# Performance work log

Hardware: AMD Instinct MI355X
Metric: run time of the kernel (lower is better)

Reference implementation:

```python
import jax, jax.numpy as jnp
import numpy as np

N = 50000      # nodes
E = 800000     # edges (avg degree 16)
DIN = 256      # input_dim
DH = 128       # hidden_dim
ALPHA_LOGIT = 0.6190392084062235  # logit(0.65)


def setup_inputs() -> dict:
    key = jax.random.key(0)
    ks = jax.random.split(key, 12)
    f = lambda k, s: jax.random.normal(k, s, dtype=jnp.float32)
    return {
        "x": f(ks[0], (N, DIN)),
        "edge_index": jax.random.randint(ks[1], (2, E), 0, N, dtype=jnp.int32),
        "reranker_scores": f(ks[2], (N,)),
        # input_proj
        "Wp": f(ks[3], (DIN, DH)) * 0.02, "bp": jnp.zeros((DH,), jnp.float32),
        # SAGEConv 0: lin_l (aggregated neighbors, with bias), lin_r (root, no bias)
        "Wl0": f(ks[4], (DIN, DH)) * 0.02, "bl0": jnp.zeros((DH,), jnp.float32),
        "Wr0": f(ks[5], (DIN, DH)) * 0.02,
        # SAGEConv 1
        "Wl1": f(ks[6], (DH, DH)) * 0.02, "bl1": jnp.zeros((DH,), jnp.float32),
        "Wr1": f(ks[7], (DH, DH)) * 0.02,
        # score head MLP
        "W1": f(ks[8], (DH, DH // 2)) * 0.02, "b1": jnp.zeros((DH // 2,), jnp.float32),
        "W2": f(ks[9], (DH // 2, 1)) * 0.02, "b2": jnp.zeros((1,), jnp.float32),
        "alpha_logit": jnp.float32(ALPHA_LOGIT),
    }


def _sage_conv(h, src, dst, Wl, bl, Wr):
    # PyG SAGEConv (aggr='mean', root_weight=True):
    # out = lin_l(mean_{j in N(i)} h_j) + lin_r(h_i)
    msg = h[src]                                             # [E, d] gather
    agg = jax.ops.segment_sum(msg, dst, num_segments=N)      # [N, d]
    cnt = jax.ops.segment_sum(jnp.ones((src.shape[0],), h.dtype), dst, num_segments=N)
    agg = agg / jnp.maximum(cnt, 1.0)[:, None]               # mean; isolated nodes -> 0
    return agg @ Wl + bl + h @ Wr


def reference(x, edge_index, reranker_scores, Wp, bp, Wl0, bl0, Wr0,
              Wl1, bl1, Wr1, W1, b1, W2, b2, alpha_logit):
    src, dst = edge_index[0], edge_index[1]
    # norm_type='none' -> no input normalization; eval mode -> dropout is identity
    residual = x @ Wp + bp                                   # [N, DH]
    h = jax.nn.relu(_sage_conv(x, src, dst, Wl0, bl0, Wr0)) + residual
    h = jax.nn.relu(_sage_conv(h, src, dst, Wl1, bl1, Wr1)) + h
    gnn_scores = (jax.nn.relu(h @ W1 + b1) @ W2 + b2)[:, 0]  # [N]
    alpha = jax.nn.sigmoid(alpha_logit)
    return alpha * reranker_scores + (1.0 - alpha) * gnn_scores
```

## Files before the change

kernel.cpp:

```cpp
#include <hip/hip_runtime.h>
#include <hip/hip_bf16.h>


#define DIN 256
#define DH 128
#define NPB 512
#define NBMAX 128
#define EPB 2048
#define JL (EPB/256)
#define CAP 12288
#define SLOTS 16384

typedef __attribute__((ext_vector_type(8))) short short8;
typedef __attribute__((ext_vector_type(4))) float float4v;
typedef __attribute__((ext_vector_type(2))) float float2v;

__device__ inline ushort f2b(float f){
  unsigned u = __float_as_uint(f);
  u = (u + 0x7fffu + ((u >> 16) & 1u)) >> 16;
  return (ushort)u;
}
__device__ inline float blo(unsigned v){ return __uint_as_float(v << 16); }
__device__ inline float bhi(unsigned v){ return __uint_as_float(v & 0xffff0000u); }
__device__ inline short8 pack8(float4 f0, float4 f1){
  short8 v;
  v[0]=(short)f2b(f0.x); v[1]=(short)f2b(f0.y); v[2]=(short)f2b(f0.z); v[3]=(short)f2b(f0.w);
  v[4]=(short)f2b(f1.x); v[5]=(short)f2b(f1.y); v[6]=(short)f2b(f1.z); v[7]=(short)f2b(f1.w);
  return v;
}
__device__ inline void glds16(const ushort* g, ushort* l){
  __builtin_amdgcn_global_load_lds((const __attribute__((address_space(1))) void*)g,
                                   (__attribute__((address_space(3))) void*)l, 16, 0, 0);
}
__device__ inline unsigned char enc8(float v){
  return (unsigned char)(__builtin_amdgcn_cvt_pk_fp8_f32(v, v, 0, false) & 0xFF);
}
__device__ inline float2v dec8(unsigned u){
  return __builtin_amdgcn_cvt_pk_f32_fp8((int)u, false);
}

__global__ __launch_bounds__(256) void fused_front(
    const float* __restrict__ x, int N, ushort* __restrict__ xb, int nstripe,
    const float* __restrict__ Wp, const float* __restrict__ Wl0, const float* __restrict__ Wr0,
    const float* __restrict__ Wl1, const float* __restrict__ Wr1, const float* __restrict__ W1,
    ushort* __restrict__ Wpf, ushort* __restrict__ Wl0f, ushort* __restrict__ Wr0f,
    ushort* __restrict__ Wl1f, ushort* __restrict__ Wr1f, ushort* __restrict__ W1f,
    const int* __restrict__ src, const int* __restrict__ dst, int E, int NB,
    int* __restrict__ bucketCnt, int* __restrict__ pairS, int* __restrict__ pairD,
    int nPart, int nConv)
{
  __shared__ int hist[NBMAX], lbase[NBMAX], gbase[NBMAX], lcur[NBMAX], sc[NBMAX];
  __shared__ int ls[EPB], ld[EPB];
  int bid = blockIdx.x;
  int t = threadIdx.x;

  if (bid < nPart){
    int base = bid * EPB;
    int cntE = E - base; if (cntE > EPB) cntE = EPB;
    for (int i=t;i<NB;i+=256) hist[i]=0;
    __syncthreads();
    int myS[JL], myD[JL];
    #pragma unroll
    for (int j=0;j<JL;j++){
      int e = base + j*256 + t;
      if (e < E){ myS[j]=src[e]; myD[j]=dst[e]; atomicAdd(&hist[myD[j]>>9],1); }
      else myD[j] = -1;
    }
    __syncthreads();
    if (t < NBMAX) sc[t] = (t < NB)? hist[t] : 0;
    __syncthreads();
    for (int st=1; st<NBMAX; st<<=1){
      int v = 0;
      if (t < NBMAX && t >= st) v = sc[t-st];
      __syncthreads();
      if (t < NBMAX) sc[t] += v;
      __syncthreads();
    }
    if (t < NB){
      int excl = (t>0)? sc[t-1] : 0;
      lbase[t] = excl; lcur[t] = excl;
      gbase[t] = atomicAdd(&bucketCnt[t], hist[t]);
    }
    __syncthreads();
    #pragma unroll
    for (int j=0;j<JL;j++){
      if (myD[j] >= 0){
        int b = myD[j] >> 9;
        int p = atomicAdd(&lcur[b], 1);
        ls[p] = myS[j]; ld[p] = myD[j];
      }
    }
    __syncthreads();
    for (int i=t;i<cntE;i+=256){
      int d = ld[i];
      int b = d >> 9;
      int p = gbase[b] + (i - lbase[b]);
      if (p < SLOTS){
        pairS[(size_t)b*SLOTS + p] = ls[i];
        pairD[(size_t)b*SLOTS + p] = d;
      }
    }
  } else if (bid < nPart + nConv){
    int gi = (bid - nPart)*256 + t;
    if (gi < nstripe*512){
      int L = gi & 63, ks = (gi>>6)&7, s = gi>>9;
      int row = s*16 + (L&15);
      int k = ks*32 + (L>>4)*8;
      short8 v;
      if (row < N){
        const float* p = x + (size_t)row*DIN + k;
        v = pack8(*(const float4*)p, *(const float4*)(p+4));
      } else {
        #pragma unroll
        for (int j=0;j<8;j++) v[j]=0;
      }
      *(short8*)(xb + (size_t)gi*8) = v;
    }
  } else {
    int gi = (bid - nPart - nConv)*256 + t;
    if (gi < 17408){
      const float* sw; ushort* dw; int cols, b0;
      if      (gi <  4096){ sw=Wp;  dw=Wpf;  cols=128; b0=0; }
      else if (gi <  8192){ sw=Wl0; dw=Wl0f; cols=128; b0=4096; }
      else if (gi < 12288){ sw=Wr0; dw=Wr0f; cols=128; b0=8192; }
      else if (gi < 14336){ sw=Wl1; dw=Wl1f; cols=128; b0=12288; }
      else if (gi < 16384){ sw=Wr1; dw=Wr1f; cols=128; b0=14336; }
      else                { sw=W1;  dw=W1f;  cols=64;  b0=16384; }
      int i = gi - b0;
      int ln = i & 63, g = i >> 6;
      int ntq = cols >> 4;
      int nt = g % ntq, ks = g / ntq;
      int col = nt*16 + (ln & 15);
      int k0 = ks*32 + (ln >> 4)*8;
      short8 v;
      #pragma unroll
      for (int j=0;j<8;j++) v[j] = (short)f2b(sw[(size_t)(k0+j)*cols + col]);
      *(short8*)(dw + (size_t)i*8) = v;
    }
  }
}

__global__ __launch_bounds__(256) void gemm0_csr(
    const ushort* __restrict__ xb, int N, int nstripe, int ngemm,
    const ushort* __restrict__ Wpf, const ushort* __restrict__ Wl0f, const ushort* __restrict__ Wr0f,
    const float* __restrict__ bp,
    ushort* __restrict__ xp, unsigned char* __restrict__ q8, ushort* __restrict__ xr0,
    const int* __restrict__ bucketCnt, const int* __restrict__ pairS, const int* __restrict__ pairD,
    int* __restrict__ off, int* __restrict__ deg, int* __restrict__ adj)
{
  __shared__ __align__(16) ushort smem[32768];
  int bid = blockIdx.x, t = threadIdx.x;

  if (bid < ngemm){
    int mat = bid % 3, b = bid / 3;
    int nblk = ngemm / 3;
    const ushort* Wf = (mat==0)? Wpf : (mat==1)? Wl0f : Wr0f;
    int w = t>>6, lane = t&63, lq = lane&15, quad = lane>>4;
    #pragma unroll
    for (int j=0;j<16;j++){
      int g = w + j*4;
      glds16(Wf + (size_t)g*512 + lane*8, smem + g*512);
    }
    __syncthreads();
    float bias[8];
    #pragma unroll
    for (int nt=0;nt<8;nt++) bias[nt] = (mat==0)? bp[nt*16 + lq] : 0.f;
    int nchunk = (nstripe + 3) >> 2;
    for (int c = b; c < nchunk; c += nblk){
      int stripe = c*4 + w;
      int row0 = stripe*16;
      if (row0 >= N) continue;
      short8 av[8];
      #pragma unroll
      for (int ks=0;ks<8;ks++)
        av[ks] = *(const short8*)(xb + ((size_t)stripe*8 + ks)*512 + lane*8);
      float4v acc[8];
      #pragma unroll
      for (int nt=0;nt<8;nt++)
        #pragma unroll
        for (int r=0;r<4;r++) acc[nt][r] = 0.f;
      #pragma unroll
      for (int ks=0;ks<8;ks++){
        #pragma unroll
        for (int nt=0;nt<8;nt++){
          short8 bf = *(const short8*)(smem + (size_t)((ks*8 + nt)*64 + lane)*8);
          acc[nt] = __builtin_amdgcn_mfma_f32_16x16x32_bf16(av[ks], bf, acc[nt], 0,0,0);
        }
      }
      if (mat == 1){
        #pragma unroll
        for (int nt=0;nt<8;nt++)
          #pragma unroll
          for (int r=0;r<4;r++){
            int row = row0 + quad*4 + r;
            if (row < N) q8[(size_t)row*128 + nt*16 + lq] = enc8(acc[nt][r]);
          }
      } else {
        ushort* Y = (mat==0)? xp : xr0;
        #pragma unroll
        for (int nt=0;nt<8;nt++)
          #pragma unroll
          for (int r=0;r<4;r++){
            int row = row0 + quad*4 + r;
            if (row < N) Y[(size_t)row*128 + nt*16 + lq] = f2b(acc[nt][r] + bias[nt]);
          }
      }
    }
  } else {
    int b = bid - ngemm;
    int* cnt  = (int*)smem;
    int* offl = cnt + NPB;
    int* s1   = offl + NPB + 1;
    int* win  = s1 + 256;
    int node0 = b * NPB;
    int base  = b * SLOTS;
    int ce = bucketCnt[b]; if (ce > SLOTS) ce = SLOTS;
    for (int i=t;i<NPB;i+=256) cnt[i]=0;
    __syncthreads();
    for (int i=t;i<ce;i+=256) atomicAdd(&cnt[pairD[(size_t)base+i]-node0], 1);
    __syncthreads();
    int a0 = cnt[2*t], a1 = cnt[2*t+1];
    s1[t] = a0 + a1;
    __syncthreads();
    for (int st=1; st<256; st<<=1){
      int v = (t>=st)? s1[t-st] : 0;
      __syncthreads();
      s1[t] += v;
      __syncthreads();
    }
    int excl = (t>0)? s1[t-1] : 0;
    offl[2*t] = excl; offl[2*t+1] = excl + a0;
    __syncthreads();
    for (int i=t;i<NPB;i+=256){
      int node = node0 + i;
      if (node < N){ off[node] = base + offl[i]; deg[node] = cnt[i]; }
    }
    __syncthreads();
    if (ce <= CAP){
      for (int i=t;i<ce;i+=256){
        int d = pairD[(size_t)base+i];
        int p = atomicAdd(&offl[d-node0], 1);
        win[p] = pairS[(size_t)base+i];
      }
      __syncthreads();
      for (int i=t;i<ce;i+=256) adj[(size_t)base+i] = win[i];
    } else {
      for (int i=t;i<ce;i+=256){
        int d = pairD[(size_t)base+i];
        int p = atomicAdd(&offl[d-node0], 1);
        adj[(size_t)base+p] = pairS[(size_t)base+i];
      }
    }
  }
}

__global__ __launch_bounds__(256) void combine0_f8(
    const unsigned char* __restrict__ agg8, const ushort* __restrict__ rootsrc,
    const ushort* __restrict__ ressrc, const float* __restrict__ bias,
    const int* __restrict__ off, const int* __restrict__ deg,
    const int* __restrict__ adj, ushort* __restrict__ out, int n)
{
  int t = threadIdx.x;
  int d = t & 63;
  int node = blockIdx.x*4 + (t >> 6);
  if (node >= n) return;
  int s = off[node], e = s + deg[node];
  const ushort* a8 = (const ushort*)agg8;
  float a0 = 0.f, a1 = 0.f;
  int p = s;
  for (; p+16 <= e; p += 16){
    ushort u[16];
    #pragma unroll
    for (int j=0;j<16;j++) u[j] = a8[(size_t)adj[p+j]*64 + d];
    #pragma unroll
    for (int j=0;j<16;j++){
      float2v f = dec8(u[j]);
      a0 += f[0]; a1 += f[1];
    }
  }
  for (; p+4 <= e; p += 4){
    ushort u0 = a8[(size_t)adj[p  ]*64 + d];
    ushort u1 = a8[(size_t)adj[p+1]*64 + d];
    ushort u2 = a8[(size_t)adj[p+2]*64 + d];
    ushort u3 = a8[(size_t)adj[p+3]*64 + d];
    float2v f0 = dec8(u0), f1 = dec8(u1), f2 = dec8(u2), f3 = dec8(u3);
    a0 += (f0[0]+f1[0]) + (f2[0]+f3[0]);
    a1 += (f0[1]+f1[1]) + (f2[1]+f3[1]);
  }
  for (; p < e; p++){
    float2v f = dec8(a8[(size_t)adj[p]*64 + d]);
    a0 += f[0]; a1 += f[1];
  }
  int cnt = e - s;
  float inv = 1.f / (float)((cnt > 1)? cnt : 1);
  unsigned rt = ((const unsigned*)rootsrc)[(size_t)node*64 + d];
  unsigned rs = ((const unsigned*)ressrc)[(size_t)node*64 + d];
  float o0 = fmaxf(a0*inv + bias[2*d]   + blo(rt), 0.f) + blo(rs);
  float o1 = fmaxf(a1*inv + bias[2*d+1] + bhi(rt), 0.f) + bhi(rs);
  ((unsigned*)out)[(size_t)node*64 + d] = (unsigned)f2b(o0) | ((unsigned)f2b(o1) << 16);
}

__global__ __launch_bounds__(256) void gemm1_wres(
    const ushort* __restrict__ h, int N,
    const ushort* __restrict__ Wl1f, const ushort* __restrict__ Wr1f,
    unsigned char* __restrict__ q8, ushort* __restrict__ hr1)
{
  __shared__ __align__(16) ushort Bs[32768];
  int t = threadIdx.x, w = t>>6, lane = t&63, lq = lane&15, quad = lane>>4;
  int tile = blockIdx.x;
  #pragma unroll
  for (int j=0;j<16;j++){
    int r = w + j*4;
    int m = r>>5, g = r&31;
    const ushort* Wm = m ? Wr1f : Wl1f;
    glds16(Wm + (size_t)g*512 + lane*8, Bs + r*512);
  }
  short8 av[2][4];
  int row0 = tile*128 + w*32;
  #pragma unroll
  for (int mt=0;mt<2;mt++){
    int row = row0 + mt*16 + lq; if (row >= N) row = N-1;
    #pragma unroll
    for (int ks=0;ks<4;ks++)
      av[mt][ks] = *(const short8*)(h + (size_t)row*128 + ks*32 + quad*8);
  }
  __syncthreads();
  #pragma unroll
  for (int m=0;m<2;m++){
    float4v acc[2][8];
    #pragma unroll
    for (int i=0;i<2;i++)
      #pragma unroll
      for (int j=0;j<8;j++)
        #pragma unroll
        for (int r=0;r<4;r++) acc[i][j][r] = 0.f;
    #pragma unroll
    for (int ks=0;ks<4;ks++){
      #pragma unroll
      for (int nt=0;nt<8;nt++){
        short8 bf = *(const short8*)(Bs + ((m*32 + ks*8 + nt)*64 + lane)*8);
        acc[0][nt] = __builtin_amdgcn_mfma_f32_16x16x32_bf16(av[0][ks], bf, acc[0][nt], 0,0,0);
        acc[1][nt] = __builtin_amdgcn_mfma_f32_16x16x32_bf16(av[1][ks], bf, acc[1][nt], 0,0,0);
      }
    }
    #pragma unroll
    for (int mt=0;mt<2;mt++){
      #pragma unroll
      for (int r=0;r<4;r++){
        int row = row0 + mt*16 + quad*4 + r;
        if (row < N){
          if (m == 0){
            #pragma unroll
            for (int nt=0;nt<8;nt++)
              q8[(size_t)row*128 + nt*16 + lq] = enc8(acc[mt][nt][r]);
          } else {
            #pragma unroll
            for (int nt=0;nt<8;nt++)
              hr1[(size_t)row*128 + nt*16 + lq] = f2b(acc[mt][nt][r]);
          }
        }
      }
    }
  }
}

__global__ __launch_bounds__(256) void combine1_head(
    const unsigned char* __restrict__ agg8, const ushort* __restrict__ hr1,
    const ushort* __restrict__ h, const float* __restrict__ bl1,
    const int* __restrict__ off, const int* __restrict__ deg, const int* __restrict__ adj,
    const ushort* __restrict__ W1f, const float* __restrict__ b1,
    const float* __restrict__ W2, const float* __restrict__ b2,
    const float* __restrict__ alogit, const float* __restrict__ rer,
    float* __restrict__ out, int n)
{
  __shared__ __align__(16) ushort W1s[8192];
  __shared__ __align__(16) ushort h2s[16*136];
  int t = threadIdx.x, w = t>>6, lane = t&63, lq = lane&15, quad = lane>>4;
  #pragma unroll
  for (int j=0;j<4;j++){
    int g = w + j*4;
    glds16(W1f + (size_t)g*512 + lane*8, W1s + g*512);
  }
  int node0 = blockIdx.x*16;
  unsigned* h2u = (unsigned*)h2s;
  const ushort* a8 = (const ushort*)agg8;
  #pragma unroll
  for (int j=0;j<4;j++){
    int node = node0 + w*4 + j;
    float o0 = 0.f, o1 = 0.f;
    if (node < n){
      int s = off[node], e = s + deg[node];
      float a0 = 0.f, a1 = 0.f;
      int p = s;
      for (; p+16 <= e; p += 16){
        ushort u[16];
        #pragma unroll
        for (int jj=0;jj<16;jj++) u[jj] = a8[(size_t)adj[p+jj]*64 + lane];
        #pragma unroll
        for (int jj=0;jj<16;jj++){
          float2v f = dec8(u[jj]);
          a0 += f[0]; a1 += f[1];
        }
      }
      for (; p+4 <= e; p += 4){
        ushort u0 = a8[(size_t)adj[p  ]*64 + lane];
        ushort u1 = a8[(size_t)adj[p+1]*64 + lane];
        ushort u2 = a8[(size_t)adj[p+2]*64 + lane];
        ushort u3 = a8[(size_t)adj[p+3]*64 + lane];
        float2v f0 = dec8(u0), f1 = dec8(u1), f2 = dec8(u2), f3 = dec8(u3);
        a0 += (f0[0]+f1[0]) + (f2[0]+f3[0]);
        a1 += (f0[1]+f1[1]) + (f2[1]+f3[1]);
      }
      for (; p < e; p++){
        float2v f = dec8(a8[(size_t)adj[p]*64 + lane]);
        a0 += f[0]; a1 += f[1];
      }
      int cnt = e - s;
      float inv = 1.f / (float)((cnt > 1)? cnt : 1);
      unsigned rt = ((const unsigned*)hr1)[(size_t)node*64 + lane];
      unsigned rs = ((const unsigned*)h)[(size_t)node*64 + lane];
      o0 = fmaxf(a0*inv + bl1[2*lane]   + blo(rt), 0.f) + blo(rs);
      o1 = fmaxf(a1*inv + bl1[2*lane+1] + bhi(rt), 0.f) + bhi(rs);
    }
    h2u[(w*4+j)*68 + lane] = (unsigned)f2b(o0) | ((unsigned)f2b(o1) << 16);
  }
  __syncthreads();

  short8 av[4];
  #pragma unroll
  for (int ks=0;ks<4;ks++)
    av[ks] = *(const short8*)(h2s + lq*136 + ks*32 + quad*8);
  float4v acc[4];
  #pragma unroll
  for (int nt=0;nt<4;nt++)
    #pragma unroll
    for (int r=0;r<4;r++) acc[nt][r] = 0.f;
  #pragma unroll
  for (int ks=0;ks<4;ks++){
    #pragma unroll
    for (int nt=0;nt<4;nt++){
      short8 bf = *(const short8*)(W1s + ((ks*4 + nt)*64 + lane)*8);
      acc[nt] = __builtin_amdgcn_mfma_f32_16x16x32_bf16(av[ks], bf, acc[nt], 0,0,0);
    }
  }
  float al = alogit[0];
  float a  = 1.f / (1.f + __expf(-al));
  float pw[4] = {0.f,0.f,0.f,0.f};
  #pragma unroll
  for (int nt=0; nt<4; nt++){
    int c = nt*16 + lq;
    float w2 = W2[c];
    float bb = b1[c];
    #pragma unroll
    for (int r=0; r<4; r++)
      pw[r] += fmaxf(acc[nt][r] + bb, 0.f) * w2;
  }
  #pragma unroll
  for (int mask=1; mask<16; mask<<=1){
    #pragma unroll
    for (int r=0; r<4; r++)
      pw[r] += __shfl_xor(pw[r], mask);
  }
  if (lq == 0){
    #pragma unroll
    for (int r=0; r<4; r++){
      int rl = quad*4 + r;
      if ((rl >> 2) == w){
        int node = node0 + rl;
        if (node < n)
          out[node] = a * rer[node] + (1.f - a) * (pw[r] + b2[0]);
      }
    }
  }
}

extern "C" void kernel_launch(void* const* d_in, const int* in_sizes, int n_in,
                              void* d_out, int out_size, void* d_ws, size_t ws_size,
                              hipStream_t stream)
{
  (void)n_in; (void)out_size; (void)ws_size;
  const float* x    = (const float*)d_in[0];
  const int*   ei   = (const int*)d_in[1];
  const float* rer  = (const float*)d_in[2];
  const float* Wp   = (const float*)d_in[3];
  const float* bp   = (const float*)d_in[4];
  const float* Wl0  = (const float*)d_in[5];
  const float* bl0  = (const float*)d_in[6];
  const float* Wr0  = (const float*)d_in[7];
  const float* Wl1  = (const float*)d_in[8];
  const float* bl1  = (const float*)d_in[9];
  const float* Wr1  = (const float*)d_in[10];
  const float* W1   = (const float*)d_in[11];
  const float* b1   = (const float*)d_in[12];
  const float* W2   = (const float*)d_in[13];
  const float* b2   = (const float*)d_in[14];
  const float* alogit = (const float*)d_in[15];

  const int N = in_sizes[2];
  const int E = in_sizes[1] / 2;
  const int* src = ei;
  const int* dst = ei + E;
  const int NB = (N + NPB - 1) / NPB;
  const int nstripe = (N + 15) / 16;
  const int ntile = (N + 127) / 128;
  const int nPart = (E + EPB - 1) / EPB;
  const int nConv = (nstripe*512 + 255)/256;

  ushort* U = (ushort*)d_ws;
  ushort* xb  = U;
  ushort* xp  = xb + (size_t)nstripe*512*8;
  ushort* xr0 = xp  + (size_t)N*DH;
  ushort* h   = xr0 + (size_t)N*DH;
  unsigned char* q8 = (unsigned char*)(h + (size_t)N*DH);
  ushort* Wpf  = (ushort*)(q8 + (size_t)N*DH);
  ushort* Wl0f = Wpf  + (size_t)4096*8;
  ushort* Wr0f = Wl0f + (size_t)4096*8;
  ushort* Wl1f = Wr0f + (size_t)4096*8;
  ushort* Wr1f = Wl1f + (size_t)2048*8;
  ushort* W1f  = Wr1f + (size_t)2048*8;
  int* I = (int*)(W1f + (size_t)1024*8);
  int* bucketCnt = I;
  int* off   = bucketCnt + NBMAX;
  int* deg   = off + N;
  int* pairS = deg + N;
  int* pairD = pairS + (size_t)NB*SLOTS;
  int* adj   = pairD + (size_t)NB*SLOTS;

  hipMemsetAsync(bucketCnt, 0, NBMAX*sizeof(int), stream);

  fused_front<<<nPart + nConv + 68, 256, 0, stream>>>(
      x, N, xb, nstripe, Wp, Wl0, Wr0, Wl1, Wr1, W1,
      Wpf, Wl0f, Wr0f, Wl1f, Wr1f, W1f,
      src, dst, E, NB, bucketCnt, pairS, pairD, nPart, nConv);

  gemm0_csr<<<768 + NB, 256, 0, stream>>>(
      xb, N, nstripe, 768, Wpf, Wl0f, Wr0f, bp, xp, q8, xr0,
      bucketCnt, pairS, pairD, off, deg, adj);

  combine0_f8<<<(N+3)/4, 256, 0, stream>>>(q8, xr0, xp, bl0, off, deg, adj, h, N);

  gemm1_wres<<<ntile, 256, 0, stream>>>(h, N, Wl1f, Wr1f, q8, xr0);

  combine1_head<<<(N+15)/16, 256, 0, stream>>>(
      q8, xr0, h, bl1, off, deg, adj, W1f, b1, W2, b2, alogit, rer, (float*)d_out, N);
}
```

Baseline: 257.0 us.

## Pad CSR rows to multiples of 16 with a zero sentinel; gather two nodes per wave

The CSR build now rounds each node's neighbor list up to a multiple of 16 and fills the padding with index N, which points at a zeroed extra row in the fp8 feature buffer. This lets both combine kernels drop their remainder loops and always run full 16-wide unrolled gathers. Each wave also interleaves the gathers of two nodes so more independent loads are in flight. In exchange, padding adds wasted loads (up to 15 per node, which is large at average degree 16), uses more bucket slots so it can overflow CAP/SLOTS more often, and reads an extra sentinel row.

```diff
diff --git a/kernel.cpp b/kernel.cpp
--- a/kernel.cpp
+++ b/kernel.cpp
@@ -37,6 +37,34 @@
 }
 __device__ inline float2v dec8(unsigned u){
   return __builtin_amdgcn_cvt_pk_f32_fp8((int)u, false);
+}
+
+__device__ inline void gather16x2(const ushort* __restrict__ a8,
+    const int* __restrict__ adj, int pA, int eA, int pB, int eB, int lane,
+    float& a0A, float& a1A, float& a0B, float& a1B)
+{
+  while (pA < eA || pB < eB){
+    ushort uA[16], uB[16];
+    bool dA = pA < eA, dB = pB < eB;
+    if (dA){
+      #pragma unroll
+      for (int j=0;j<16;j++) uA[j] = a8[(size_t)adj[pA+j]*64 + lane];
+    }
+    if (dB){
+      #pragma unroll
+      for (int j=0;j<16;j++) uB[j] = a8[(size_t)adj[pB+j]*64 + lane];
+    }
+    if (dA){
+      #pragma unroll
+      for (int j=0;j<16;j++){ float2v f = dec8(uA[j]); a0A += f[0]; a1A += f[1]; }
+      pA += 16;
+    }
+    if (dB){
+      #pragma unroll
+      for (int j=0;j<16;j++){ float2v f = dec8(uB[j]); a0B += f[0]; a1B += f[1]; }
+      pB += 16;
+    }
+  }
 }
 
 __global__ __launch_bounds__(256) void fused_front(
@@ -220,7 +248,9 @@
     for (int i=t;i<ce;i+=256) atomicAdd(&cnt[pairD[(size_t)base+i]-node0], 1);
     __syncthreads();
     int a0 = cnt[2*t], a1 = cnt[2*t+1];
-    s1[t] = a0 + a1;
+    int p0 = (a0 + 15) & ~15;
+    int p1 = (a1 + 15) & ~15;
+    s1[t] = p0 + p1;
     __syncthreads();
     for (int st=1; st<256; st<<=1){
       int v = (t>=st)? s1[t-st] : 0;
@@ -229,26 +259,31 @@
       __syncthreads();
     }
     int excl = (t>0)? s1[t-1] : 0;
-    offl[2*t] = excl; offl[2*t+1] = excl + a0;
+    offl[2*t] = excl; offl[2*t+1] = excl + p0;
+    int ptotal = s1[255]; if (ptotal > SLOTS) ptotal = SLOTS;
     __syncthreads();
     for (int i=t;i<NPB;i+=256){
       int node = node0 + i;
       if (node < N){ off[node] = base + offl[i]; deg[node] = cnt[i]; }
     }
     __syncthreads();
-    if (ce <= CAP){
+    if (ptotal <= CAP){
+      for (int i=t;i<ptotal;i+=256) win[i] = N;
+      __syncthreads();
       for (int i=t;i<ce;i+=256){
-        int d = pairD[(size_t)base+i];
-        int p = atomicAdd(&offl[d-node0], 1);
+        int dd = pairD[(size_t)base+i];
+        int p = atomicAdd(&offl[dd-node0], 1);
         win[p] = pairS[(size_t)base+i];
       }
       __syncthreads();
-      for (int i=t;i<ce;i+=256) adj[(size_t)base+i] = win[i];
+      for (int i=t;i<ptotal;i+=256) adj[(size_t)base+i] = win[i];
     } else {
+      for (int i=t;i<ptotal;i+=256) adj[(size_t)base+i] = N;
+      __syncthreads();
       for (int i=t;i<ce;i+=256){
-        int d = pairD[(size_t)base+i];
-        int p = atomicAdd(&offl[d-node0], 1);
-        adj[(size_t)base+p] = pairS[(size_t)base+i];
+        int dd = pairD[(size_t)base+i];
+        int p = atomicAdd(&offl[dd-node0], 1);
+        if (p < SLOTS) adj[(size_t)base+p] = pairS[(size_t)base+i];
       }
     }
   }
@@ -261,43 +296,34 @@
     const int* __restrict__ adj, ushort* __restrict__ out, int n)
 {
   int t = threadIdx.x;
-  int d = t & 63;
-  int node = blockIdx.x*4 + (t >> 6);
-  if (node >= n) return;
-  int s = off[node], e = s + deg[node];
+  int d = t & 63, w = t >> 6;
+  int nA = blockIdx.x*8 + w*2, nB = nA + 1;
+  if (nA >= n) return;
   const ushort* a8 = (const ushort*)agg8;
-  float a0 = 0.f, a1 = 0.f;
-  int p = s;
-  for (; p+16 <= e; p += 16){
-    ushort u[16];
-    #pragma unroll
-    for (int j=0;j<16;j++) u[j] = a8[(size_t)adj[p+j]*64 + d];
-    #pragma unroll
-    for (int j=0;j<16;j++){
-      float2v f = dec8(u[j]);
-      a0 += f[0]; a1 += f[1];
-    }
-  }
-  for (; p+4 <= e; p += 4){
-    ushort u0 = a8[(size_t)adj[p  ]*64 + d];
-    ushort u1 = a8[(size_t)adj[p+1]*64 + d];
-    ushort u2 = a8[(size_t)adj[p+2]*64 + d];
-    ushort u3 = a8[(size_t)adj[p+3]*64 + d];
-    float2v f0 = dec8(u0), f1 = dec8(u1), f2 = dec8(u2), f3 = dec8(u3);
-    a0 += (f0[0]+f1[0]) + (f2[0]+f3[0]);
-    a1 += (f0[1]+f1[1]) + (f2[1]+f3[1]);
-  }
-  for (; p < e; p++){
-    float2v f = dec8(a8[(size_t)adj[p]*64 + d]);
-    a0 += f[0]; a1 += f[1];
-  }
-  int cnt = e - s;
-  float inv = 1.f / (float)((cnt > 1)? cnt : 1);
-  unsigned rt = ((const unsigned*)rootsrc)[(size_t)node*64 + d];
-  unsigned rs = ((const unsigned*)ressrc)[(size_t)node*64 + d];
-  float o0 = fmaxf(a0*inv + bias[2*d]   + blo(rt), 0.f) + blo(rs);
-  float o1 = fmaxf(a1*inv + bias[2*d+1] + bhi(rt), 0.f) + bhi(rs);
-  ((unsigned*)out)[(size_t)node*64 + d] = (unsigned)f2b(o0) | ((unsigned)f2b(o1) << 16);
+  bool vB = nB < n;
+  unsigned rtA = ((const unsigned*)rootsrc)[(size_t)nA*64 + d];
+  unsigned rsA = ((const unsigned*)ressrc)[(size_t)nA*64 + d];
+  unsigned rtB = 0, rsB = 0;
+  int pA = off[nA], cA = deg[nA], eA = pA + ((cA + 15) & ~15);
+  int pB = 0, cB = 0, eB = 0;
+  if (vB){
+    rtB = ((const unsigned*)rootsrc)[(size_t)nB*64 + d];
+    rsB = ((const unsigned*)ressrc)[(size_t)nB*64 + d];
+    pB = off[nB]; cB = deg[nB]; eB = pB + ((cB + 15) & ~15);
+  }
+  float a0A=0.f, a1A=0.f, a0B=0.f, a1B=0.f;
+  gather16x2(a8, adj, pA, eA, pB, eB, d, a0A, a1A, a0B, a1B);
+  float b0 = bias[2*d], b1v = bias[2*d+1];
+  float invA = 1.f / (float)((cA > 1)? cA : 1);
+  float o0 = fmaxf(a0A*invA + b0  + blo(rtA), 0.f) + blo(rsA);
+  float o1 = fmaxf(a1A*invA + b1v + bhi(rtA), 0.f) + bhi(rsA);
+  ((unsigned*)out)[(size_t)nA*64 + d] = (unsigned)f2b(o0) | ((unsigned)f2b(o1) << 16);
+  if (vB){
+    float invB = 1.f / (float)((cB > 1)? cB : 1);
+    float q0 = fmaxf(a0B*invB + b0  + blo(rtB), 0.f) + blo(rsB);
+    float q1 = fmaxf(a1B*invB + b1v + bhi(rtB), 0.f) + bhi(rsB);
+    ((unsigned*)out)[(size_t)nB*64 + d] = (unsigned)f2b(q0) | ((unsigned)f2b(q1) << 16);
+  }
 }
 
 __global__ __launch_bounds__(256) void gemm1_wres(
@@ -384,45 +410,38 @@
   int node0 = blockIdx.x*16;
   unsigned* h2u = (unsigned*)h2s;
   const ushort* a8 = (const ushort*)agg8;
-  #pragma unroll
-  for (int j=0;j<4;j++){
-    int node = node0 + w*4 + j;
-    float o0 = 0.f, o1 = 0.f;
-    if (node < n){
-      int s = off[node], e = s + deg[node];
-      float a0 = 0.f, a1 = 0.f;
-      int p = s;
-      for (; p+16 <= e; p += 16){
-        ushort u[16];
-        #pragma unroll
-        for (int jj=0;jj<16;jj++) u[jj] = a8[(size_t)adj[p+jj]*64 + lane];
-        #pragma unroll
-        for (int jj=0;jj<16;jj++){
-          float2v f = dec8(u[jj]);
-          a0 += f[0]; a1 += f[1];
-        }
-      }
-      for (; p+4 <= e; p += 4){
-        ushort u0 = a8[(size_t)adj[p  ]*64 + lane];
-        ushort u1 = a8[(size_t)adj[p+1]*64 + lane];
-        ushort u2 = a8[(size_t)adj[p+2]*64 + lane];
-        ushort u3 = a8[(size_t)adj[p+3]*64 + lane];
-        float2v f0 = dec8(u0), f1 = dec8(u1), f2 = dec8(u2), f3 = dec8(u3);
-        a0 += (f0[0]+f1[0]) + (f2[0]+f3[0]);
-        a1 += (f0[1]+f1[1]) + (f2[1]+f3[1]);
-      }
-      for (; p < e; p++){
-        float2v f = dec8(a8[(size_t)adj[p]*64 + lane]);
-        a0 += f[0]; a1 += f[1];
-      }
-      int cnt = e - s;
-      float inv = 1.f / (float)((cnt > 1)? cnt : 1);
-      unsigned rt = ((const unsigned*)hr1)[(size_t)node*64 + lane];
-      unsigned rs = ((const unsigned*)h)[(size_t)node*64 + lane];
-      o0 = fmaxf(a0*inv + bl1[2*lane]   + blo(rt), 0.f) + blo(rs);
-      o1 = fmaxf(a1*inv + bl1[2*lane+1] + bhi(rt), 0.f) + bhi(rs);
-    }
-    h2u[(w*4+j)*68 + lane] = (unsigned)f2b(o0) | ((unsigned)f2b(o1) << 16);
+  float bb0 = bl1[2*lane], bb1 = bl1[2*lane+1];
+  #pragma unroll
+  for (int jp=0;jp<2;jp++){
+    int nA = node0 + w*4 + jp*2, nB = nA + 1;
+    bool vA = nA < n, vB = nB < n;
+    unsigned rtA=0, rsA=0, rtB=0, rsB=0;
+    int pA=0, eA=0, cA=0, pB=0, eB=0, cB=0;
+    if (vA){
+      rtA = ((const unsigned*)hr1)[(size_t)nA*64 + lane];
+      rsA = ((const unsigned*)h  )[(size_t)nA*64 + lane];
+      pA = off[nA]; cA = deg[nA]; eA = pA + ((cA + 15) & ~15);
+    }
+    if (vB){
+      rtB = ((const unsigned*)hr1)[(size_t)nB*64 + lane];
+      rsB = ((const unsigned*)h  )[(size_t)nB*64 + lane];
+      pB = off[nB]; cB = deg[nB]; eB = pB + ((cB + 15) & ~15);
+    }
+    float a0A=0.f, a1A=0.f, a0B=0.f, a1B=0.f;
+    gather16x2(a8, adj, pA, eA, pB, eB, lane, a0A, a1A, a0B, a1B);
+    float o0A=0.f, o1A=0.f, o0B=0.f, o1B=0.f;
+    if (vA){
+      float inv = 1.f / (float)((cA > 1)? cA : 1);
+      o0A = fmaxf(a0A*inv + bb0 + blo(rtA), 0.f) + blo(rsA);
+      o1A = fmaxf(a1A*inv + bb1 + bhi(rtA), 0.f) + bhi(rsA);
+    }
+    if (vB){
+      float inv = 1.f / (float)((cB > 1)? cB : 1);
+      o0B = fmaxf(a0B*inv + bb0 + blo(rtB), 0.f) + blo(rsB);
+      o1B = fmaxf(a1B*inv + bb1 + bhi(rtB), 0.f) + bhi(rsB);
+    }
+    h2u[(w*4 + jp*2    )*68 + lane] = (unsigned)f2b(o0A) | ((unsigned)f2b(o1A) << 16);
+    h2u[(w*4 + jp*2 + 1)*68 + lane] = (unsigned)f2b(o0B) | ((unsigned)f2b(o1B) << 16);
   }
   __syncthreads();
 
@@ -512,7 +531,7 @@
   ushort* xr0 = xp  + (size_t)N*DH;
   ushort* h   = xr0 + (size_t)N*DH;
   unsigned char* q8 = (unsigned char*)(h + (size_t)N*DH);
-  ushort* Wpf  = (ushort*)(q8 + (size_t)N*DH);
+  ushort* Wpf  = (ushort*)(q8 + (size_t)(N+1)*DH);
   ushort* Wl0f = Wpf  + (size_t)4096*8;
   ushort* Wr0f = Wl0f + (size_t)4096*8;
   ushort* Wl1f = Wr0f + (size_t)4096*8;
@@ -527,6 +546,7 @@
   int* adj   = pairD + (size_t)NB*SLOTS;
 
   hipMemsetAsync(bucketCnt, 0, NBMAX*sizeof(int), stream);
+  hipMemsetAsync(q8 + (size_t)N*DH, 0, DH, stream);
 
   fused_front<<<nPart + nConv + 68, 256, 0, stream>>>(
       x, N, xb, nstripe, Wp, Wl0, Wr0, Wl1, Wr1, W1,
@@ -537,7 +557,7 @@
       xb, N, nstripe, 768, Wpf, Wl0f, Wr0f, bp, xp, q8, xr0,
       bucketCnt, pairS, pairD, off, deg, adj);
 
-  combine0_f8<<<(N+3)/4, 256, 0, stream>>>(q8, xr0, xp, bl0, off, deg, adj, h, N);
+  combine0_f8<<<(N+7)/8, 256, 0, stream>>>(q8, xr0, xp, bl0, off, deg, adj, h, N);
 
   gemm1_wres<<<ntile, 256, 0, stream>>>(h, N, Wl1f, Wr1f, q8, xr0);
 
```

After: 250.2 us. -2.6%, faster.
